# Performance work log

Hardware: AMD Instinct MI355X
Metric: run time of the kernel (lower is better)

## Reference

```python
import jax, jax.numpy as jnp
import numpy as np

NUM_LAYERS, NUM_HEADS, HEAD_DIM = 12, 12, 64
D = NUM_HEADS * HEAD_DIM  # 768
VOCAB, MAX_POS = 50257, 1024
BLOCK_SIZE, NUM_BLOCKS = 16, 128
SEQ_LEN = 1024
EPS = 1e-5
SCALE = 1.0 / float(np.sqrt(HEAD_DIM))


def layer_norm(x, g, b):
    m = jnp.mean(x, axis=-1, keepdims=True)
    v = jnp.var(x, axis=-1, keepdims=True)
    return (x - m) * jax.lax.rsqrt(v + EPS) * g + b


def setup_inputs() -> dict:
    key = jax.random.key(0)
    ks = jax.random.split(key, 12)
    p = lambda k, shape: jax.random.normal(k, shape, jnp.float32) * 0.02
    Lyr = NUM_LAYERS
    return {
        "input_ids": jax.random.randint(ks[0], (SEQ_LEN,), 0, VOCAB, dtype=jnp.int32),
        "start_pos": 0,
        "block_ids": jnp.arange(SEQ_LEN // BLOCK_SIZE, dtype=jnp.int32),
        "kv_k_pool": jnp.zeros((Lyr, NUM_BLOCKS, BLOCK_SIZE, NUM_HEADS, HEAD_DIM), jnp.float32),
        "kv_v_pool": jnp.zeros((Lyr, NUM_BLOCKS, BLOCK_SIZE, NUM_HEADS, HEAD_DIM), jnp.float32),
        "wte": p(ks[1], (VOCAB, D)),
        "wpe": p(ks[2], (MAX_POS, D)),
        "ln1_g": jnp.ones((Lyr, D), jnp.float32),
        "ln1_b": jnp.zeros((Lyr, D), jnp.float32),
        "attn_w": p(ks[3], (Lyr, D, 3 * D)),
        "attn_b": jnp.zeros((Lyr, 3 * D), jnp.float32),
        "attn_pw": p(ks[4], (Lyr, D, D)),
        "attn_pb": jnp.zeros((Lyr, D), jnp.float32),
        "ln2_g": jnp.ones((Lyr, D), jnp.float32),
        "ln2_b": jnp.zeros((Lyr, D), jnp.float32),
        "fc_w": p(ks[5], (Lyr, D, 4 * D)),
        "fc_b": jnp.zeros((Lyr, 4 * D), jnp.float32),
        "proj_w": p(ks[6], (Lyr, 4 * D, D)),
        "proj_b": jnp.zeros((Lyr, D), jnp.float32),
        "lnf_g": jnp.ones((D,), jnp.float32),
        "lnf_b": jnp.zeros((D,), jnp.float32),
    }


def reference(input_ids, start_pos, block_ids, kv_k_pool, kv_v_pool, wte, wpe,
              ln1_g, ln1_b, attn_w, attn_b, attn_pw, attn_pb, ln2_g, ln2_b,
              fc_w, fc_b, proj_w, proj_b, lnf_g, lnf_b):
    L = input_ids.shape[0]
    T = start_pos + L  # total cached tokens after this step
    positions = start_pos + jnp.arange(L)

    x = wte[input_ids] + wpe[positions]  # [L, D]

    # paged cache index maps: logical pos -> (physical block, offset)
    w_blk = block_ids[positions // BLOCK_SIZE]
    w_off = positions % BLOCK_SIZE
    r_pos = jnp.arange(T)
    r_blk = block_ids[r_pos // BLOCK_SIZE]
    r_off = r_pos % BLOCK_SIZE

    causal_mask = r_pos[None, :] > positions[:, None]  # [L, T]

    for i in range(NUM_LAYERS):
        h = layer_norm(x, ln1_g[i], ln1_b[i])
        qkv = h @ attn_w[i] + attn_b[i]  # [L, 3D]
        q, k, v = jnp.split(qkv, 3, axis=-1)
        q = q.reshape(L, NUM_HEADS, HEAD_DIM)
        k = k.reshape(L, NUM_HEADS, HEAD_DIM)
        v = v.reshape(L, NUM_HEADS, HEAD_DIM)

        # kv_pool.write: scatter new K/V rows into block-indexed slots
        kv_k_pool = kv_k_pool.at[i, w_blk, w_off].set(k)
        kv_v_pool = kv_v_pool.at[i, w_blk, w_off].set(v)
        # kv_pool.read: gather first T logical tokens through block table
        k_cache = kv_k_pool[i, r_blk, r_off]  # [T, H, d]
        v_cache = kv_v_pool[i, r_blk, r_off]  # [T, H, d]

        scores = jnp.einsum('lhd,thd->hlt', q, k_cache) * SCALE  # [H, L, T]
        scores = jnp.where(causal_mask[None, :, :], -jnp.inf, scores)
        attn = jax.nn.softmax(scores.astype(jnp.float32), axis=-1).astype(scores.dtype)
        out = jnp.einsum('hlt,thd->lhd', attn, v_cache).reshape(L, D)
        x = x + out @ attn_pw[i] + attn_pb[i]

        h2 = layer_norm(x, ln2_g[i], ln2_b[i])
        x = x + jax.nn.gelu(h2 @ fc_w[i] + fc_b[i], approximate=True) @ proj_w[i] + proj_b[i]

    x = layer_norm(x, lnf_g, lnf_b)
    logits = x @ wte.T  # [L, V]
    return logits
```

## Files before the change

kernel.cpp:

```cpp
#include <hip/hip_runtime.h>
#include <math.h>


#define SEQ 1024
#define DMODEL 768
#define NHEADS 12
#define HEADD 64
#define ATT_SCALE 0.125f

typedef unsigned short u16;
typedef __bf16 bf16x8 __attribute__((ext_vector_type(8)));
typedef float f32x4 __attribute__((ext_vector_type(4)));

__device__ __forceinline__ u16 bf(float f) {
    return __builtin_bit_cast(u16, (__bf16)f);
}

__device__ __forceinline__ void gll16(const u16* g, u16* l) {
    __builtin_amdgcn_global_load_lds(
        (const __attribute__((address_space(1))) unsigned int*)g,
        (__attribute__((address_space(3))) unsigned int*)l, 16, 0, 0);
}

template <int MODE, bool GELU, bool BOUND>
__global__ __launch_bounds__(256) void gemm_bt(
    const u16* __restrict__ A, int lda, long aBatch,
    const u16* __restrict__ B, int ldb, long bBatch,
    void* __restrict__ Cv, int ldc, long cBatch,
    const float* __restrict__ bias, int N, int K) {
    __shared__ alignas(16) u16 As[64 * 64];
    __shared__ alignas(16) u16 Bs[64 * 64];

    const int z = blockIdx.z;
    A += (long)z * aBatch;
    B += (long)z * bBatch;

    const int m0 = blockIdx.x * 64;
    const int n0 = blockIdx.y * 64;
    const int t = threadIdx.x;

    const int srow = t >> 3;
    const int scol = ((t & 7) ^ (srow & 7)) << 3;

    const u16* aSrc0 = A + (long)(m0 + srow) * lda + scol;
    const u16* aSrc1 = A + (long)(m0 + srow + 32) * lda + scol;
    int br0 = n0 + srow, br1 = n0 + srow + 32;
    if (BOUND) {
        if (br0 > N - 1) br0 = N - 1;
        if (br1 > N - 1) br1 = N - 1;
    }
    const u16* bSrc0 = B + (long)br0 * ldb + scol;
    const u16* bSrc1 = B + (long)br1 * ldb + scol;

    u16* aDst = &As[t * 8];
    u16* bDst = &Bs[t * 8];

    const int lane = t & 63, w = t >> 6;
    const int quad = lane >> 4, ml = lane & 15;
    const int sw = ml & 7;
    const int arow64 = (w * 16 + ml) * 64;

    f32x4 acc[4] = {f32x4{0, 0, 0, 0}, f32x4{0, 0, 0, 0},
                    f32x4{0, 0, 0, 0}, f32x4{0, 0, 0, 0}};

    for (int k0 = 0; k0 < K; k0 += 64) {
        if (k0) __syncthreads();
        gll16(aSrc0, aDst);
        gll16(aSrc1, aDst + 2048);
        gll16(bSrc0, bDst);
        gll16(bSrc1, bDst + 2048);
        aSrc0 += 64; aSrc1 += 64; bSrc0 += 64; bSrc1 += 64;
        __syncthreads();

        bf16x8 a0 = *(const bf16x8*)&As[arow64 + ((quad ^ sw) << 3)];
        bf16x8 a1 = *(const bf16x8*)&As[arow64 + (((4 + quad) ^ sw) << 3)];
#pragma unroll
        for (int i = 0; i < 4; ++i) {
            const int brow64 = (i * 16 + ml) * 64;
            bf16x8 b0 = *(const bf16x8*)&Bs[brow64 + ((quad ^ sw) << 3)];
            bf16x8 b1 = *(const bf16x8*)&Bs[brow64 + (((4 + quad) ^ sw) << 3)];
            acc[i] = __builtin_amdgcn_mfma_f32_16x16x32_bf16(a0, b0, acc[i], 0, 0, 0);
            acc[i] = __builtin_amdgcn_mfma_f32_16x16x32_bf16(a1, b1, acc[i], 0, 0, 0);
        }
    }

    float* Cf = (float*)Cv + (MODE != 1 ? (long)z * cBatch : 0);
    u16*   Ch = (u16*)Cv  + (MODE == 1 ? (long)z * cBatch : 0);
    const int mrow = m0 + w * 16 + quad * 4;
#pragma unroll
    for (int i = 0; i < 4; ++i) {
        const int col = n0 + i * 16 + ml;
        if (BOUND && col >= N) continue;
        const float bv = bias ? bias[col] : 0.f;
#pragma unroll
        for (int r = 0; r < 4; ++r) {
            float v = acc[i][r] + bv;
            if (GELU) {
                v = 0.5f * v * (1.f + tanhf(0.7978845608028654f * (v + 0.044715f * v * v * v)));
            }
            const long idx = (long)(mrow + r) * ldc + col;
            if (MODE == 0)      Cf[idx] = v;
            else if (MODE == 1) Ch[idx] = bf(v);
            else                Cf[idx] += v;
        }
    }
}

__global__ __launch_bounds__(256) void wtrans4_kernel(
    const float* __restrict__ aw, const float* __restrict__ apw,
    const float* __restrict__ fw, const float* __restrict__ pw,
    u16* __restrict__ awT, u16* __restrict__ apwT,
    u16* __restrict__ fwT, u16* __restrict__ pwT) {
    int b = blockIdx.x;
    const float* src; u16* dst; int K, N;
    if (b < 432)       { src = aw;  dst = awT;  K = 768;  N = 2304; }
    else if (b < 576)  { src = apw; dst = apwT; K = 768;  N = 768;  b -= 432; }
    else if (b < 1152) { src = fw;  dst = fwT;  K = 768;  N = 3072; b -= 576; }
    else               { src = pw;  dst = pwT;  K = 3072; N = 768;  b -= 1152; }
    const int ntn = N >> 6;
    const int n0 = (b % ntn) << 6, k0 = (b / ntn) << 6;

    __shared__ u16 tile[64][68];
    const int t = threadIdx.x, r = t >> 2, c0 = (t & 3) << 4;

    const float* srow = src + (long)(k0 + r) * N + n0 + c0;
    u16* trow = &tile[r][c0];
#pragma unroll
    for (int j = 0; j < 16; ++j) trow[j] = bf(srow[j]);
    __syncthreads();

    alignas(16) u16 tmp[16];
#pragma unroll
    for (int j = 0; j < 16; ++j) tmp[j] = tile[c0 + j][r];
    u16* drow = dst + (long)(n0 + r) * K + k0 + c0;
    *(uint4*)drow       = *(const uint4*)tmp;
    *(uint4*)(drow + 8) = *(const uint4*)(tmp + 8);
}

__global__ __launch_bounds__(256) void vtrans_kernel(
    const u16* __restrict__ qkvb, u16* __restrict__ vT) {
    const int t0 = blockIdx.x << 6, h = blockIdx.y;
    __shared__ u16 tile[64][68];
    const int t = threadIdx.x, r = t >> 2, c0 = (t & 3) << 4;
    const u16* srow = qkvb + (long)(t0 + r) * (3 * DMODEL) + 2 * DMODEL + h * HEADD + c0;
#pragma unroll
    for (int j = 0; j < 16; ++j) tile[r][c0 + j] = srow[j];
    __syncthreads();
    alignas(16) u16 tmp[16];
#pragma unroll
    for (int j = 0; j < 16; ++j) tmp[j] = tile[c0 + j][r];
    u16* drow = vT + ((long)h * HEADD + r) * SEQ + t0 + c0;
    *(uint4*)drow       = *(const uint4*)tmp;
    *(uint4*)(drow + 8) = *(const uint4*)(tmp + 8);
}

__global__ __launch_bounds__(256) void cvt_bf16_kernel(
    const float* __restrict__ src, u16* __restrict__ dst, long n8) {
    const float4* sp = (const float4*)src;
    for (long i = blockIdx.x * 256 + threadIdx.x; i < n8; i += (long)gridDim.x * 256) {
        const float4 a = sp[2 * i], b = sp[2 * i + 1];
        alignas(16) u16 o[8] = {bf(a.x), bf(a.y), bf(a.z), bf(a.w),
                                bf(b.x), bf(b.y), bf(b.z), bf(b.w)};
        ((uint4*)dst)[i] = *(const uint4*)o;
    }
}

__device__ inline float wave_sum(float v) {
#pragma unroll
    for (int o = 32; o > 0; o >>= 1) v += __shfl_xor(v, o, 64);
    return v;
}
__device__ inline float wave_max(float v) {
#pragma unroll
    for (int o = 32; o > 0; o >>= 1) v = fmaxf(v, __shfl_xor(v, o, 64));
    return v;
}
__device__ inline float block_sum(float v, float* red) {
    v = wave_sum(v);
    if ((threadIdx.x & 63) == 0) red[threadIdx.x >> 6] = v;
    __syncthreads();
    v = red[0] + red[1] + red[2] + red[3];
    __syncthreads();
    return v;
}
__device__ inline float block_max(float v, float* red) {
    v = wave_max(v);
    if ((threadIdx.x & 63) == 0) red[threadIdx.x >> 6] = v;
    __syncthreads();
    v = fmaxf(fmaxf(red[0], red[1]), fmaxf(red[2], red[3]));
    __syncthreads();
    return v;
}

__global__ __launch_bounds__(256) void embed_kernel(
    const int* __restrict__ ids, const float* __restrict__ wte,
    const float* __restrict__ wpe, float* __restrict__ x) {
    const int l = blockIdx.x;
    const long wo = (long)ids[l] * DMODEL;
    const long po = (long)l * DMODEL;
#pragma unroll
    for (int j = 0; j < 3; ++j) {
        const int d = threadIdx.x + j * 256;
        x[po + d] = wte[wo + d] + wpe[po + d];
    }
}

__global__ __launch_bounds__(256) void ln_kernel(
    const float* __restrict__ x, const float* __restrict__ g,
    const float* __restrict__ b, u16* __restrict__ out) {
    __shared__ float red[4];
    const int row = blockIdx.x;
    const float* xr = x + (long)row * DMODEL;
    const int t = threadIdx.x;
    float v0 = xr[t], v1 = xr[t + 256], v2 = xr[t + 512];
    const float mean = block_sum(v0 + v1 + v2, red) * (1.f / DMODEL);
    const float d0 = v0 - mean, d1 = v1 - mean, d2 = v2 - mean;
    const float var = block_sum(d0 * d0 + d1 * d1 + d2 * d2, red) * (1.f / DMODEL);
    const float inv = rsqrtf(var + 1e-5f);
    u16* orow = out + (long)row * DMODEL;
    orow[t]       = bf(d0 * inv * g[t]       + b[t]);
    orow[t + 256] = bf(d1 * inv * g[t + 256] + b[t + 256]);
    orow[t + 512] = bf(d2 * inv * g[t + 512] + b[t + 512]);
}

__global__ __launch_bounds__(256) void softmax_kernel(
    const float* __restrict__ scores, u16* __restrict__ P) {
    __shared__ float red[4];
    const int l = blockIdx.x, h = blockIdx.y;
    const long row = (long)h * SEQ + l;
    const float4 s4 = ((const float4*)(scores + row * SEQ))[threadIdx.x];
    const int base = threadIdx.x * 4;
    const float e0 = (base + 0 <= l) ? s4.x * ATT_SCALE : -1e30f;
    const float e1 = (base + 1 <= l) ? s4.y * ATT_SCALE : -1e30f;
    const float e2 = (base + 2 <= l) ? s4.z * ATT_SCALE : -1e30f;
    const float e3 = (base + 3 <= l) ? s4.w * ATT_SCALE : -1e30f;
    const float mx = block_max(fmaxf(fmaxf(e0, e1), fmaxf(e2, e3)), red);
    const float p0 = expf(e0 - mx), p1 = expf(e1 - mx);
    const float p2 = expf(e2 - mx), p3 = expf(e3 - mx);
    const float inv = 1.f / block_sum(p0 + p1 + p2 + p3, red);
    alignas(8) u16 o[4] = {bf(p0 * inv), bf(p1 * inv), bf(p2 * inv), bf(p3 * inv)};
    *(uint2*)(P + row * SEQ + base) = *(const uint2*)o;
}

extern "C" void kernel_launch(void* const* d_in, const int* in_sizes, int n_in,
                              void* d_out, int out_size, void* d_ws, size_t ws_size,
                              hipStream_t stream) {
    const int* input_ids = (const int*)d_in[0];
    const float* wte     = (const float*)d_in[5];
    const float* wpe     = (const float*)d_in[6];
    const float* ln1_g   = (const float*)d_in[7];
    const float* ln1_b   = (const float*)d_in[8];
    const float* attn_w  = (const float*)d_in[9];
    const float* attn_b  = (const float*)d_in[10];
    const float* attn_pw = (const float*)d_in[11];
    const float* attn_pb = (const float*)d_in[12];
    const float* ln2_g   = (const float*)d_in[13];
    const float* ln2_b   = (const float*)d_in[14];
    const float* fc_w    = (const float*)d_in[15];
    const float* fc_b    = (const float*)d_in[16];
    const float* proj_w  = (const float*)d_in[17];
    const float* proj_b  = (const float*)d_in[18];
    const float* lnf_g   = (const float*)d_in[19];
    const float* lnf_b   = (const float*)d_in[20];

    char* p = (char*)d_ws;
    auto carve = [&](long bytes) { char* q = p; p += (bytes + 255) & ~255L; return q; };
    float* x     = (float*)carve((long)SEQ * DMODEL * 4);
    u16*  hbf    = (u16*)carve((long)SEQ * DMODEL * 2);
    u16*  qkvb   = (u16*)carve((long)SEQ * 3 * DMODEL * 2);
    u16*  vT     = (u16*)carve((long)NHEADS * HEADD * SEQ * 2);
    u16*  awT    = (u16*)carve((long)2304 * 768 * 2);
    u16*  apwT   = (u16*)carve((long)768 * 768 * 2);
    u16*  fwT    = (u16*)carve((long)3072 * 768 * 2);
    u16*  pwT    = (u16*)carve((long)768 * 3072 * 2);
    char* region = p;
    float* scores = (float*)carve((long)NHEADS * SEQ * SEQ * 4);
    u16*  P      = (u16*)carve((long)NHEADS * SEQ * SEQ * 2);
    u16*  attno  = (u16*)carve((long)SEQ * DMODEL * 2);
    u16*  fcact  = (u16*)carve((long)SEQ * 4 * DMODEL * 2);
    u16*  wteBF  = (u16*)region;

    embed_kernel<<<SEQ, 256, 0, stream>>>(input_ids, wte, wpe, x);

    for (int i = 0; i < 12; ++i) {
        const float* aw  = attn_w  + (long)i * DMODEL * 3 * DMODEL;
        const float* ab  = attn_b  + (long)i * 3 * DMODEL;
        const float* apw = attn_pw + (long)i * DMODEL * DMODEL;
        const float* apb = attn_pb + (long)i * DMODEL;
        const float* fw  = fc_w    + (long)i * DMODEL * 4 * DMODEL;
        const float* fb  = fc_b    + (long)i * 4 * DMODEL;
        const float* pw  = proj_w  + (long)i * 4 * DMODEL * DMODEL;
        const float* pb  = proj_b  + (long)i * DMODEL;

        wtrans4_kernel<<<1728, 256, 0, stream>>>(aw, apw, fw, pw, awT, apwT, fwT, pwT);

        ln_kernel<<<SEQ, 256, 0, stream>>>(x, ln1_g + i * DMODEL, ln1_b + i * DMODEL, hbf);
        gemm_bt<1, false, false><<<dim3(16, 36, 1), 256, 0, stream>>>(
            hbf, DMODEL, 0, awT, DMODEL, 0, qkvb, 3 * DMODEL, 0, ab, 3 * DMODEL, DMODEL);
        vtrans_kernel<<<dim3(16, NHEADS), 256, 0, stream>>>(qkvb, vT);
        gemm_bt<0, false, false><<<dim3(16, 16, NHEADS), 256, 0, stream>>>(
            qkvb, 3 * DMODEL, HEADD, qkvb + DMODEL, 3 * DMODEL, HEADD,
            scores, SEQ, (long)SEQ * SEQ, nullptr, SEQ, HEADD);
        softmax_kernel<<<dim3(SEQ, NHEADS), 256, 0, stream>>>(scores, P);
        gemm_bt<1, false, false><<<dim3(16, 1, NHEADS), 256, 0, stream>>>(
            P, SEQ, (long)SEQ * SEQ, vT, SEQ, (long)HEADD * SEQ,
            attno, DMODEL, HEADD, nullptr, HEADD, SEQ);
        gemm_bt<2, false, false><<<dim3(16, 12, 1), 256, 0, stream>>>(
            attno, DMODEL, 0, apwT, DMODEL, 0, x, DMODEL, 0, apb, DMODEL, DMODEL);
        ln_kernel<<<SEQ, 256, 0, stream>>>(x, ln2_g + i * DMODEL, ln2_b + i * DMODEL, hbf);
        gemm_bt<1, true, false><<<dim3(16, 48, 1), 256, 0, stream>>>(
            hbf, DMODEL, 0, fwT, DMODEL, 0, fcact, 4 * DMODEL, 0, fb, 4 * DMODEL, DMODEL);
        gemm_bt<2, false, false><<<dim3(16, 12, 1), 256, 0, stream>>>(
            fcact, 4 * DMODEL, 0, pwT, 4 * DMODEL, 0, x, DMODEL, 0, pb, DMODEL, 4 * DMODEL);
    }

    ln_kernel<<<SEQ, 256, 0, stream>>>(x, lnf_g, lnf_b, hbf);
    cvt_bf16_kernel<<<2048, 256, 0, stream>>>(wte, wteBF, (long)50257 * 768 / 8);
    gemm_bt<0, false, true><<<dim3(16, 786, 1), 256, 0, stream>>>(
        hbf, DMODEL, 0, wteBF, DMODEL, 0, (float*)d_out, 50257, 0, nullptr, 50257, DMODEL);
}
```

Measured before the change: 2.261 ms.

## Fuse attention into a flash-style kernel and add 128x128 tiled logits GEMM

Replaces the separate QK^T score GEMM, softmax kernel and PV GEMM with a single flash-attention kernel. It uses an online softmax with causal tile skipping, so the full fp32 score matrix and the bf16 probability matrix are never written to or read from memory. Separately, the final vocabulary projection moves to a new 128x128-tile GEMM with XOR-swizzled LDS and a remapped workgroup order for better operand reuse. The flash kernel reads K and V straight from global memory with no LDS staging and runs only 192 workgroups, so parallelism is limited and causal load is imbalanced across query tiles.

Result: slower. 2.550 ms (+12.8%).

```diff
diff --git a/kernel.cpp b/kernel.cpp
--- a/kernel.cpp
+++ b/kernel.cpp
@@ -103,6 +103,171 @@
             else if (MODE == 1) Ch[idx] = bf(v);
             else                Cf[idx] += v;
         }
+    }
+}
+
+__global__ __launch_bounds__(256) void gemm_bt128(
+    const u16* __restrict__ A, int lda,
+    const u16* __restrict__ B, int ldb,
+    float* __restrict__ C, int ldc,
+    const float* __restrict__ bias, int N, int K) {
+    __shared__ alignas(16) u16 As[128 * 64];
+    __shared__ alignas(16) u16 Bs[128 * 64];
+
+    const int nwg = gridDim.x * gridDim.y;
+    const int lid = blockIdx.x + gridDim.x * blockIdx.y;
+    const int per = nwg >> 3;
+    const int nl  = (lid & 7) * per + (lid >> 3);
+    const int m0 = (nl & 7) << 7;
+    const int n0 = (nl >> 3) << 7;
+
+    const int t = threadIdx.x;
+    const int srow = t >> 3;
+    const int scol = ((t & 7) ^ (srow & 7)) << 3;
+
+    const u16* aS = A + (long)(m0 + srow) * lda + scol;
+    int brow[4];
+#pragma unroll
+    for (int j = 0; j < 4; ++j) {
+        int rr = n0 + srow + 32 * j;
+        brow[j] = rr < N ? rr : N - 1;
+    }
+
+    const int lane = t & 63, w = t >> 6;
+    const int quad = lane >> 4, ml = lane & 15;
+    const int wm = w >> 1, wn = w & 1, sw = ml & 7;
+
+    f32x4 acc[4][4];
+#pragma unroll
+    for (int a = 0; a < 4; ++a)
+#pragma unroll
+        for (int b = 0; b < 4; ++b) acc[a][b] = f32x4{0, 0, 0, 0};
+
+    for (int k0 = 0; k0 < K; k0 += 64) {
+        if (k0) __syncthreads();
+#pragma unroll
+        for (int j = 0; j < 4; ++j) {
+            gll16(aS + (long)(32 * j) * lda + k0, &As[t * 8 + j * 2048]);
+            gll16(B + (long)brow[j] * ldb + k0 + scol, &Bs[t * 8 + j * 2048]);
+        }
+        __syncthreads();
+#pragma unroll
+        for (int kh = 0; kh < 2; ++kh) {
+            const int so = ((kh * 4 + quad) ^ sw) << 3;
+            bf16x8 af[4], bfr[4];
+#pragma unroll
+            for (int mi = 0; mi < 4; ++mi)
+                af[mi] = *(const bf16x8*)&As[(wm * 64 + mi * 16 + ml) * 64 + so];
+#pragma unroll
+            for (int ni = 0; ni < 4; ++ni)
+                bfr[ni] = *(const bf16x8*)&Bs[(wn * 64 + ni * 16 + ml) * 64 + so];
+#pragma unroll
+            for (int mi = 0; mi < 4; ++mi)
+#pragma unroll
+                for (int ni = 0; ni < 4; ++ni)
+                    acc[mi][ni] = __builtin_amdgcn_mfma_f32_16x16x32_bf16(
+                        af[mi], bfr[ni], acc[mi][ni], 0, 0, 0);
+        }
+    }
+
+#pragma unroll
+    for (int mi = 0; mi < 4; ++mi) {
+        const int mrow = m0 + wm * 64 + mi * 16 + quad * 4;
+#pragma unroll
+        for (int ni = 0; ni < 4; ++ni) {
+            const int col = n0 + wn * 64 + ni * 16 + ml;
+            if (col >= N) continue;
+            const float bv = bias ? bias[col] : 0.f;
+#pragma unroll
+            for (int r = 0; r < 4; ++r)
+                C[(long)(mrow + r) * ldc + col] = acc[mi][ni][r] + bv;
+        }
+    }
+}
+
+__global__ __launch_bounds__(256) void fattn_kernel(
+    const u16* __restrict__ qkvb, const u16* __restrict__ vT,
+    u16* __restrict__ attno) {
+    __shared__ alignas(16) u16 Pl[4 * 16 * 72];
+    const int qt = blockIdx.x, h = blockIdx.y;
+    const int q0 = qt << 6;
+    const int t = threadIdx.x, lane = t & 63, w = t >> 6;
+    const int quad = lane >> 4, ml = lane & 15;
+
+    const long qr0 = (long)(q0 + w * 16 + ml) * (3 * DMODEL) + h * 64;
+    const bf16x8 qa0 = *(const bf16x8*)&qkvb[qr0 + quad * 8];
+    const bf16x8 qa1 = *(const bf16x8*)&qkvb[qr0 + 32 + quad * 8];
+
+    f32x4 o[4] = {f32x4{0, 0, 0, 0}, f32x4{0, 0, 0, 0},
+                  f32x4{0, 0, 0, 0}, f32x4{0, 0, 0, 0}};
+    float mrow[4] = {-1e30f, -1e30f, -1e30f, -1e30f};
+    float lrow[4] = {0.f, 0.f, 0.f, 0.f};
+
+    u16* Pw = &Pl[w * 16 * 72];
+    const int nt = qt + 1;
+
+    for (int kt = 0; kt < nt; ++kt) {
+        const int kv0 = kt << 6;
+        f32x4 s[4];
+#pragma unroll
+        for (int i = 0; i < 4; ++i) {
+            const long kr = (long)(kv0 + i * 16 + ml) * (3 * DMODEL) + DMODEL + h * 64;
+            bf16x8 kb0 = *(const bf16x8*)&qkvb[kr + quad * 8];
+            bf16x8 kb1 = *(const bf16x8*)&qkvb[kr + 32 + quad * 8];
+            f32x4 z = {0, 0, 0, 0};
+            z = __builtin_amdgcn_mfma_f32_16x16x32_bf16(qa0, kb0, z, 0, 0, 0);
+            z = __builtin_amdgcn_mfma_f32_16x16x32_bf16(qa1, kb1, z, 0, 0, 0);
+            s[i] = z;
+        }
+        const bool diag = (kt == nt - 1);
+#pragma unroll
+        for (int r = 0; r < 4; ++r) {
+            float sv[4];
+#pragma unroll
+            for (int i = 0; i < 4; ++i) sv[i] = s[i][r] * ATT_SCALE;
+            if (diag) {
+                const int qr = q0 + w * 16 + quad * 4 + r;
+#pragma unroll
+                for (int i = 0; i < 4; ++i)
+                    if (kv0 + i * 16 + ml > qr) sv[i] = -1e30f;
+            }
+            float mx = fmaxf(fmaxf(sv[0], sv[1]), fmaxf(sv[2], sv[3]));
+#pragma unroll
+            for (int msk = 1; msk < 16; msk <<= 1)
+                mx = fmaxf(mx, __shfl_xor(mx, msk, 64));
+            const float mnew = fmaxf(mrow[r], mx);
+            const float corr = expf(mrow[r] - mnew);
+            mrow[r] = mnew;
+            const float p0 = expf(sv[0] - mnew), p1 = expf(sv[1] - mnew);
+            const float p2 = expf(sv[2] - mnew), p3 = expf(sv[3] - mnew);
+            float rs = (p0 + p1) + (p2 + p3);
+#pragma unroll
+            for (int msk = 1; msk < 16; msk <<= 1)
+                rs += __shfl_xor(rs, msk, 64);
+            lrow[r] = lrow[r] * corr + rs;
+#pragma unroll
+            for (int i = 0; i < 4; ++i) o[i][r] *= corr;
+            u16* pr = Pw + (quad * 4 + r) * 72 + ml;
+            pr[0] = bf(p0); pr[16] = bf(p1); pr[32] = bf(p2); pr[48] = bf(p3);
+        }
+        const bf16x8 pa0 = *(const bf16x8*)&Pw[ml * 72 + quad * 8];
+        const bf16x8 pa1 = *(const bf16x8*)&Pw[ml * 72 + 32 + quad * 8];
+#pragma unroll
+        for (int i = 0; i < 4; ++i) {
+            const long vr = (long)(h * 64 + i * 16 + ml) * SEQ + kv0;
+            bf16x8 vb0 = *(const bf16x8*)&vT[vr + quad * 8];
+            bf16x8 vb1 = *(const bf16x8*)&vT[vr + 32 + quad * 8];
+            o[i] = __builtin_amdgcn_mfma_f32_16x16x32_bf16(pa0, vb0, o[i], 0, 0, 0);
+            o[i] = __builtin_amdgcn_mfma_f32_16x16x32_bf16(pa1, vb1, o[i], 0, 0, 0);
+        }
+    }
+
+#pragma unroll
+    for (int r = 0; r < 4; ++r) {
+        const float inv = 1.f / lrow[r];
+        u16* orow = attno + (long)(q0 + w * 16 + quad * 4 + r) * DMODEL + h * 64;
+#pragma unroll
+        for (int i = 0; i < 4; ++i) orow[i * 16 + ml] = bf(o[i][r] * inv);
     }
 }
 
@@ -170,24 +335,11 @@
     for (int o = 32; o > 0; o >>= 1) v += __shfl_xor(v, o, 64);
     return v;
 }
-__device__ inline float wave_max(float v) {
-#pragma unroll
-    for (int o = 32; o > 0; o >>= 1) v = fmaxf(v, __shfl_xor(v, o, 64));
-    return v;
-}
 __device__ inline float block_sum(float v, float* red) {
     v = wave_sum(v);
     if ((threadIdx.x & 63) == 0) red[threadIdx.x >> 6] = v;
     __syncthreads();
     v = red[0] + red[1] + red[2] + red[3];
-    __syncthreads();
-    return v;
-}
-__device__ inline float block_max(float v, float* red) {
-    v = wave_max(v);
-    if ((threadIdx.x & 63) == 0) red[threadIdx.x >> 6] = v;
-    __syncthreads();
-    v = fmaxf(fmaxf(red[0], red[1]), fmaxf(red[2], red[3]));
     __syncthreads();
     return v;
 }
@@ -221,25 +373,6 @@
     orow[t]       = bf(d0 * inv * g[t]       + b[t]);
     orow[t + 256] = bf(d1 * inv * g[t + 256] + b[t + 256]);
     orow[t + 512] = bf(d2 * inv * g[t + 512] + b[t + 512]);
-}
-
-__global__ __launch_bounds__(256) void softmax_kernel(
-    const float* __restrict__ scores, u16* __restrict__ P) {
-    __shared__ float red[4];
-    const int l = blockIdx.x, h = blockIdx.y;
-    const long row = (long)h * SEQ + l;
-    const float4 s4 = ((const float4*)(scores + row * SEQ))[threadIdx.x];
-    const int base = threadIdx.x * 4;
-    const float e0 = (base + 0 <= l) ? s4.x * ATT_SCALE : -1e30f;
-    const float e1 = (base + 1 <= l) ? s4.y * ATT_SCALE : -1e30f;
-    const float e2 = (base + 2 <= l) ? s4.z * ATT_SCALE : -1e30f;
-    const float e3 = (base + 3 <= l) ? s4.w * ATT_SCALE : -1e30f;
-    const float mx = block_max(fmaxf(fmaxf(e0, e1), fmaxf(e2, e3)), red);
-    const float p0 = expf(e0 - mx), p1 = expf(e1 - mx);
-    const float p2 = expf(e2 - mx), p3 = expf(e3 - mx);
-    const float inv = 1.f / block_sum(p0 + p1 + p2 + p3, red);
-    alignas(8) u16 o[4] = {bf(p0 * inv), bf(p1 * inv), bf(p2 * inv), bf(p3 * inv)};
-    *(uint2*)(P + row * SEQ + base) = *(const uint2*)o;
 }
 
 extern "C" void kernel_launch(void* const* d_in, const int* in_sizes, int n_in,
@@ -265,20 +398,18 @@
 
     char* p = (char*)d_ws;
     auto carve = [&](long bytes) { char* q = p; p += (bytes + 255) & ~255L; return q; };
-    float* x     = (float*)carve((long)SEQ * DMODEL * 4);
-    u16*  hbf    = (u16*)carve((long)SEQ * DMODEL * 2);
-    u16*  qkvb   = (u16*)carve((long)SEQ * 3 * DMODEL * 2);
-    u16*  vT     = (u16*)carve((long)NHEADS * HEADD * SEQ * 2);
-    u16*  awT    = (u16*)carve((long)2304 * 768 * 2);
-    u16*  apwT   = (u16*)carve((long)768 * 768 * 2);
-    u16*  fwT    = (u16*)carve((long)3072 * 768 * 2);
-    u16*  pwT    = (u16*)carve((long)768 * 3072 * 2);
+    float* x   = (float*)carve((long)SEQ * DMODEL * 4);
+    u16* hbf   = (u16*)carve((long)SEQ * DMODEL * 2);
+    u16* qkvb  = (u16*)carve((long)SEQ * 3 * DMODEL * 2);
+    u16* vT    = (u16*)carve((long)NHEADS * HEADD * SEQ * 2);
+    u16* awT   = (u16*)carve((long)2304 * 768 * 2);
+    u16* apwT  = (u16*)carve((long)768 * 768 * 2);
+    u16* fwT   = (u16*)carve((long)3072 * 768 * 2);
+    u16* pwT   = (u16*)carve((long)768 * 3072 * 2);
     char* region = p;
-    float* scores = (float*)carve((long)NHEADS * SEQ * SEQ * 4);
-    u16*  P      = (u16*)carve((long)NHEADS * SEQ * SEQ * 2);
-    u16*  attno  = (u16*)carve((long)SEQ * DMODEL * 2);
-    u16*  fcact  = (u16*)carve((long)SEQ * 4 * DMODEL * 2);
-    u16*  wteBF  = (u16*)region;
+    u16* attno = (u16*)carve((long)SEQ * DMODEL * 2);
+    u16* fcact = (u16*)carve((long)SEQ * 4 * DMODEL * 2);
+    u16* wteBF = (u16*)region;
 
     embed_kernel<<<SEQ, 256, 0, stream>>>(input_ids, wte, wpe, x);
 
@@ -298,13 +429,7 @@
         gemm_bt<1, false, false><<<dim3(16, 36, 1), 256, 0, stream>>>(
             hbf, DMODEL, 0, awT, DMODEL, 0, qkvb, 3 * DMODEL, 0, ab, 3 * DMODEL, DMODEL);
         vtrans_kernel<<<dim3(16, NHEADS), 256, 0, stream>>>(qkvb, vT);
-        gemm_bt<0, false, false><<<dim3(16, 16, NHEADS), 256, 0, stream>>>(
-            qkvb, 3 * DMODEL, HEADD, qkvb + DMODEL, 3 * DMODEL, HEADD,
-            scores, SEQ, (long)SEQ * SEQ, nullptr, SEQ, HEADD);
-        softmax_kernel<<<dim3(SEQ, NHEADS), 256, 0, stream>>>(scores, P);
-        gemm_bt<1, false, false><<<dim3(16, 1, NHEADS), 256, 0, stream>>>(
-            P, SEQ, (long)SEQ * SEQ, vT, SEQ, (long)HEADD * SEQ,
-            attno, DMODEL, HEADD, nullptr, HEADD, SEQ);
+        fattn_kernel<<<dim3(16, NHEADS), 256, 0, stream>>>(qkvb, vT, attno);
         gemm_bt<2, false, false><<<dim3(16, 12, 1), 256, 0, stream>>>(
             attno, DMODEL, 0, apwT, DMODEL, 0, x, DMODEL, 0, apb, DMODEL, DMODEL);
         ln_kernel<<<SEQ, 256, 0, stream>>>(x, ln2_g + i * DMODEL, ln2_b + i * DMODEL, hbf);
@@ -316,6 +441,6 @@
 
     ln_kernel<<<SEQ, 256, 0, stream>>>(x, lnf_g, lnf_b, hbf);
     cvt_bf16_kernel<<<2048, 256, 0, stream>>>(wte, wteBF, (long)50257 * 768 / 8);
-    gemm_bt<0, false, true><<<dim3(16, 786, 1), 256, 0, stream>>>(
-        hbf, DMODEL, 0, wteBF, DMODEL, 0, (float*)d_out, 50257, 0, nullptr, 50257, DMODEL);
-}
+    gemm_bt128<<<dim3(8, 393), 256, 0, stream>>>(
+        hbf, DMODEL, wteBF, DMODEL, (float*)d_out, 50257, nullptr, 50257, DMODEL);
+}
```
